# Performance work log

Hardware: AMD Instinct MI355X
Metric: run time of the kernel (lower is better)

## Reference

```python
import jax, jax.numpy as jnp
import numpy as np

NEG_INF = -9e15  # matches torch's -9000000000000000.0 mask value
ALPHA = 0.2      # LeakyReLU negative slope


def setup_inputs() -> dict:
    key = jax.random.key(0)
    k1, k2, k3, k4 = jax.random.split(key, 4)
    B, N, Fin, Fout, H = 32, 512, 256, 64, 8
    x = jax.random.normal(k1, (B, N, Fin), dtype=jnp.float32)
    adj = (jax.random.uniform(k2, (B, N, N)) < 0.5).astype(jnp.float32)
    # W: Linear(in_features, out_features*n_heads, bias=False) weight, stored as (Fin, Fout*H)
    W = jax.random.normal(k3, (Fin, Fout * H), dtype=jnp.float32) / np.sqrt(Fin).astype(np.float32)
    # a: attention vector per head over concat(src,dst) features -> (H, 2*Fout)
    a = jax.random.normal(k4, (H, 2 * Fout), dtype=jnp.float32) * 0.1
    return {"x": x, "adj": adj, "W": W, "a": a}


def reference(x, adj, W, a):
    # x: (B,N,Fin), adj: (B,N,N), W: (Fin, H*F), a: (H, 2F)
    B, N, _ = x.shape
    H, twoF = a.shape
    F = twoF // 2
    h = (x @ W).reshape(B, N, H, F)  # (B,N,H,F)
    # Decompose concat-score: e_ij = lrelu(h_i . a_src + h_j . a_dst) -- same math
    # as (cat(h_i,h_j) * a).sum(-1) without materializing (B,N,N,H,2F).
    s_src = jnp.einsum('bnhf,hf->bnh', h, a[:, :F])  # (B,N,H)
    s_dst = jnp.einsum('bnhf,hf->bnh', h, a[:, F:])  # (B,N,H)
    e = s_src[:, :, None, :] + s_dst[:, None, :, :]  # (B,N,N,H)
    e = jax.nn.leaky_relu(e, negative_slope=ALPHA)
    e = jnp.where(adj[..., None] > 0, e, NEG_INF)
    attn = jax.nn.softmax(e, axis=2)  # softmax over neighbors j (dim=2)
    # dropout omitted (eval mode / p effectively 0 for the reference baseline)
    h_prime = jnp.einsum('bijh,bjhf->bihf', attn, h)  # (B,N,H,F)
    return h_prime.reshape(B, N, H * F)  # concat=True
```

## Files before the change

kernel.cpp:

```cpp
#include <hip/hip_runtime.h>
#include <hip/hip_bf16.h>


#define ALPHA 0.2f

typedef __bf16 bf16x8 __attribute__((ext_vector_type(8)));
typedef __bf16 bf16x4 __attribute__((ext_vector_type(4)));
typedef float  f32x4  __attribute__((ext_vector_type(4)));

#define HT_STRIDE 520
#define WT_STRIDE 40

struct Smem {
    __bf16 hT[64][HT_STRIDE];
    __bf16 WT[64][WT_STRIDE];
    float  ssrc[512], sdst[512];
    float  rsum[256];
    float  asrc[64], adst[64];
};

__device__ inline bf16x8 ld8(const float* p) {
    float4 a0 = *(const float4*)p;
    float4 a1 = *(const float4*)(p + 4);
    bf16x8 r;
    r[0]=(__bf16)a0.x; r[1]=(__bf16)a0.y; r[2]=(__bf16)a0.z; r[3]=(__bf16)a0.w;
    r[4]=(__bf16)a1.x; r[5]=(__bf16)a1.y; r[6]=(__bf16)a1.z; r[7]=(__bf16)a1.w;
    return r;
}

__global__ __launch_bounds__(512, 4) void k_gat(const float* __restrict__ x,
                                                const float* __restrict__ adj,
                                                const float* __restrict__ W,
                                                const float* __restrict__ a,
                                                float* __restrict__ out) {
    __shared__ Smem sm;
    const int ihalf = blockIdx.x, h = blockIdx.y, b = blockIdx.z;
    const int tid  = threadIdx.x;
    const int wave = tid >> 6, lane = tid & 63;
    const int quad = lane >> 4, col = lane & 15;

    if (tid < 128) {
        float v = a[h * 128 + tid];
        if (tid < 64) sm.asrc[tid] = v; else sm.adst[tid - 64] = v;
    }

    {
        const float* xb = x + (long)b * 512 * 256;
        f32x4 acc[4][4] = {};
        const int c = tid & 63, kl = tid >> 6;
        for (int ks = 0; ks < 8; ++ks) {
            #pragma unroll
            for (int t = 0; t < 4; ++t)
                sm.WT[c][kl + t * 8] = (__bf16)W[(long)(ks * 32 + kl + t * 8) * 512 + h * 64 + c];
            __syncthreads();
            bf16x8 av[4], bv[4];
            #pragma unroll
            for (int it = 0; it < 4; ++it)
                av[it] = ld8(xb + (long)(wave * 64 + it * 16 + col) * 256 + ks * 32 + quad * 8);
            #pragma unroll
            for (int nt = 0; nt < 4; ++nt)
                bv[nt] = *(const bf16x8*)(&sm.WT[nt * 16 + col][quad * 8]);
            #pragma unroll
            for (int it = 0; it < 4; ++it)
                #pragma unroll
                for (int nt = 0; nt < 4; ++nt)
                    acc[it][nt] = __builtin_amdgcn_mfma_f32_16x16x32_bf16(av[it], bv[nt], acc[it][nt], 0, 0, 0);
            __syncthreads();
        }
        #pragma unroll
        for (int it = 0; it < 4; ++it)
            #pragma unroll
            for (int nt = 0; nt < 4; ++nt) {
                int f = nt * 16 + col;
                int j = wave * 64 + it * 16 + quad * 4;
                bf16x4 pk = { (__bf16)acc[it][nt][0], (__bf16)acc[it][nt][1],
                              (__bf16)acc[it][nt][2], (__bf16)acc[it][nt][3] };
                *(bf16x4*)(&sm.hT[f][j]) = pk;
            }
    }
    __syncthreads();

    {
        float as = 0.f, ad = 0.f;
        #pragma unroll 8
        for (int f = 0; f < 64; ++f) {
            float v = (float)sm.hT[f][tid];
            as += v * sm.asrc[f];
            ad += v * sm.adst[f];
        }
        sm.ssrc[tid] = as;
        sm.sdst[tid] = ad;
    }
    __syncthreads();

    {
        float si[2], sacc[2] = {0.f, 0.f};
        const float* arow[2];
        #pragma unroll
        for (int it = 0; it < 2; ++it) {
            int i = ihalf * 256 + wave * 32 + it * 16 + col;
            si[it]   = sm.ssrc[i & 511];
            arow[it] = adj + ((long)(b * 512 + i)) * 512;
        }
        f32x4 acc[2][4] = {};
        for (int ks = 0; ks < 16; ++ks) {
            int j0 = ks * 32 + quad * 8;
            f32x4 s0 = *(const f32x4*)&sm.sdst[j0];
            f32x4 s1 = *(const f32x4*)&sm.sdst[j0 + 4];
            float sd[8] = {s0[0],s0[1],s0[2],s0[3],s1[0],s1[1],s1[2],s1[3]};
            bf16x8 P[2];
            #pragma unroll
            for (int it = 0; it < 2; ++it) {
                float4 a0 = *(const float4*)(arow[it] + j0);
                float4 a1 = *(const float4*)(arow[it] + j0 + 4);
                float am[8] = {a0.x,a0.y,a0.z,a0.w,a1.x,a1.y,a1.z,a1.w};
                #pragma unroll
                for (int u = 0; u < 8; ++u) {
                    float e = si[it] + sd[u];
                    e = e > 0.f ? e : ALPHA * e;
                    float p = (am[u] > 0.f) ? __expf(e) : 0.f;
                    __bf16 pb = (__bf16)p;
                    sacc[it] += (float)pb;
                    P[it][u] = pb;
                }
            }
            #pragma unroll
            for (int nt = 0; nt < 4; ++nt) {
                bf16x8 bv = *(const bf16x8*)(&sm.hT[nt * 16 + col][j0]);
                #pragma unroll
                for (int it = 0; it < 2; ++it)
                    acc[it][nt] = __builtin_amdgcn_mfma_f32_16x16x32_bf16(P[it], bv, acc[it][nt], 0, 0, 0);
            }
        }
        #pragma unroll
        for (int it = 0; it < 2; ++it) {
            float s = sacc[it];
            s += __shfl_xor(s, 16);
            s += __shfl_xor(s, 32);
            if (quad == 0) sm.rsum[wave * 32 + it * 16 + col] = s;
        }
        __syncthreads();
        #pragma unroll
        for (int it = 0; it < 2; ++it)
            #pragma unroll
            for (int r = 0; r < 4; ++r) {
                int li = wave * 32 + it * 16 + quad * 4 + r;
                int i  = ihalf * 256 + li;
                float s = sm.rsum[li];
                float inv = (s > 0.f) ? 1.0f / s : 0.f;
                float* orow = out + ((long)(b * 512 + i)) * 512 + h * 64;
                #pragma unroll
                for (int nt = 0; nt < 4; ++nt)
                    orow[nt * 16 + col] = acc[it][nt][r] * inv;
            }
    }
}

extern "C" void kernel_launch(void* const* d_in, const int* in_sizes, int n_in,
                              void* d_out, int out_size, void* d_ws, size_t ws_size,
                              hipStream_t stream) {
    const float* x   = (const float*)d_in[0];
    const float* adj = (const float*)d_in[1];
    const float* W   = (const float*)d_in[2];
    const float* a   = (const float*)d_in[3];
    float* out = (float*)d_out;
    (void)d_ws; (void)ws_size;

    k_gat<<<dim3(2, 8, 32), 512, 0, stream>>>(x, adj, W, a, out);
}
```

Measured before the change: 161.0 us.

## Split GAT into projection and attention kernels through workspace, one block per head

Splits the fused kernel into two kernels. The first computes h = xW once per (batch, head), stores it transposed in bf16 in workspace, and folds the source and destination scores into the MFMA epilogue. The second loads h into XOR-swizzled shared memory and handles all 512 rows per block, where the old kernel recomputed the projection for each half of the rows. It also uses exp2 with prescaled scores, multiplies by the adjacency value instead of branching, and gets row sums from an MFMA against a ones vector. A fused fallback remains for small workspaces, and the split costs an extra launch plus roughly 17 MB of workspace traffic.

```diff
diff --git a/kernel.cpp b/kernel.cpp
--- a/kernel.cpp
+++ b/kernel.cpp
@@ -8,16 +8,13 @@
 typedef __bf16 bf16x4 __attribute__((ext_vector_type(4)));
 typedef float  f32x4  __attribute__((ext_vector_type(4)));
 
-#define HT_STRIDE 520
-#define WT_STRIDE 40
-
-struct Smem {
-    __bf16 hT[64][HT_STRIDE];
-    __bf16 WT[64][WT_STRIDE];
-    float  ssrc[512], sdst[512];
-    float  rsum[256];
-    float  asrc[64], adst[64];
-};
+#if __has_builtin(__builtin_amdgcn_exp2f)
+#define EXP2(x) __builtin_amdgcn_exp2f(x)
+#define ESCALE  1.4426950408889634f
+#else
+#define EXP2(x) __expf(x)
+#define ESCALE  1.0f
+#endif
 
 __device__ inline bf16x8 ld8(const float* p) {
     float4 a0 = *(const float4*)p;
@@ -28,44 +25,215 @@
     return r;
 }
 
-__global__ __launch_bounds__(512, 4) void k_gat(const float* __restrict__ x,
-                                                const float* __restrict__ adj,
-                                                const float* __restrict__ W,
-                                                const float* __restrict__ a,
-                                                float* __restrict__ out) {
-    __shared__ Smem sm;
-    const int ihalf = blockIdx.x, h = blockIdx.y, b = blockIdx.z;
-    const int tid  = threadIdx.x;
+#define WT_STRIDE 264
+__global__ __launch_bounds__(512) void k_h(const float* __restrict__ x,
+                                           const float* __restrict__ W,
+                                           const float* __restrict__ a,
+                                           __bf16* __restrict__ hT,
+                                           float* __restrict__ ssrc,
+                                           float* __restrict__ sdst) {
+    __shared__ __bf16 WT[64][WT_STRIDE];
+    const int h = blockIdx.x, b = blockIdx.y;
+    const int tid = threadIdx.x;
     const int wave = tid >> 6, lane = tid & 63;
     const int quad = lane >> 4, col = lane & 15;
-
+    const long bh = b * 8 + h;
+
+    {
+        int c = tid & 63, k0 = tid >> 6;
+        #pragma unroll 4
+        for (int t = 0; t < 32; ++t)
+            WT[c][k0 + t * 8] = (__bf16)W[(long)(k0 + t * 8) * 512 + h * 64 + c];
+    }
+    float asv[4], adv[4];
+    #pragma unroll
+    for (int nt = 0; nt < 4; ++nt) {
+        asv[nt] = a[h * 128 + nt * 16 + col];
+        adv[nt] = a[h * 128 + 64 + nt * 16 + col];
+    }
+    __syncthreads();
+
+    const float* xb = x + (long)b * 512 * 256;
+    f32x4 acc[4][4] = {};
+    for (int ks = 0; ks < 8; ++ks) {
+        int k0 = ks * 32 + quad * 8;
+        bf16x8 av[4], bv[4];
+        #pragma unroll
+        for (int it = 0; it < 4; ++it)
+            av[it] = ld8(xb + (long)(wave * 64 + it * 16 + col) * 256 + k0);
+        #pragma unroll
+        for (int nt = 0; nt < 4; ++nt)
+            bv[nt] = *(const bf16x8*)(&WT[nt * 16 + col][k0]);
+        #pragma unroll
+        for (int it = 0; it < 4; ++it)
+            #pragma unroll
+            for (int nt = 0; nt < 4; ++nt)
+                acc[it][nt] = __builtin_amdgcn_mfma_f32_16x16x32_bf16(av[it], bv[nt], acc[it][nt], 0, 0, 0);
+    }
+    #pragma unroll
+    for (int it = 0; it < 4; ++it)
+        #pragma unroll
+        for (int nt = 0; nt < 4; ++nt) {
+            int f = nt * 16 + col;
+            int j = wave * 64 + it * 16 + quad * 4;
+            bf16x4 pk = { (__bf16)acc[it][nt][0], (__bf16)acc[it][nt][1],
+                          (__bf16)acc[it][nt][2], (__bf16)acc[it][nt][3] };
+            *(bf16x4*)(hT + (bh * 64 + f) * 512 + j) = pk;
+        }
+    #pragma unroll
+    for (int it = 0; it < 4; ++it)
+        #pragma unroll
+        for (int r = 0; r < 4; ++r) {
+            float ps = 0.f, pd = 0.f;
+            #pragma unroll
+            for (int nt = 0; nt < 4; ++nt) {
+                ps += acc[it][nt][r] * asv[nt];
+                pd += acc[it][nt][r] * adv[nt];
+            }
+            #pragma unroll
+            for (int off = 1; off < 16; off <<= 1) {
+                ps += __shfl_xor(ps, off);
+                pd += __shfl_xor(pd, off);
+            }
+            if (col == 0) {
+                int j = wave * 64 + it * 16 + quad * 4 + r;
+                ssrc[bh * 512 + j] = ps * ESCALE;
+                sdst[bh * 512 + j] = pd * ESCALE;
+            }
+        }
+}
+
+__global__ __launch_bounds__(512, 4) void k_attn(const float* __restrict__ adj,
+                                                 const __bf16* __restrict__ hT,
+                                                 const float* __restrict__ ssrc,
+                                                 const float* __restrict__ sdst,
+                                                 float* __restrict__ out) {
+    __shared__ __bf16 hTs[64 * 512];
+    __shared__ float  sdsts[512], ssrcs[512];
+    const int h = blockIdx.x, b = blockIdx.y;
+    const int tid = threadIdx.x;
+    const int wave = tid >> 6, lane = tid & 63;
+    const int quad = lane >> 4, col = lane & 15;
+    const long bh = b * 8 + h;
+
+    {
+        int f = tid >> 3, c8 = tid & 7, s = f & 7;
+        const __bf16* src = hT + (bh * 64 + f) * 512;
+        #pragma unroll
+        for (int k = 0; k < 8; ++k) {
+            int blk = k * 8 + c8;
+            *(float4*)(&hTs[f * 512 + ((blk ^ s) * 8)]) = *(const float4*)(src + blk * 8);
+        }
+    }
+    ssrcs[tid] = ssrc[bh * 512 + tid];
+    sdsts[tid] = sdst[bh * 512 + tid];
+    __syncthreads();
+
+    float si[4];
+    const float* arow[4];
+    #pragma unroll
+    for (int it = 0; it < 4; ++it) {
+        int i = wave * 64 + it * 16 + col;
+        si[it]   = ssrcs[i];
+        arow[it] = adj + ((long)b * 512 + i) * 512;
+    }
+    bf16x8 ones;
+    #pragma unroll
+    for (int u = 0; u < 8; ++u) ones[u] = (__bf16)1.0f;
+
+    f32x4 acc[4][4] = {};
+    f32x4 accs[4]   = {};
+    for (int ks = 0; ks < 16; ++ks) {
+        int j0 = ks * 32 + quad * 8;
+        f32x4 s0 = *(const f32x4*)&sdsts[j0];
+        f32x4 s1 = *(const f32x4*)&sdsts[j0 + 4];
+        float sd[8] = {s0[0],s0[1],s0[2],s0[3],s1[0],s1[1],s1[2],s1[3]};
+        bf16x8 bv[4];
+        int sblk = ((ks * 4 + quad) ^ (col & 7)) * 8;
+        #pragma unroll
+        for (int nt = 0; nt < 4; ++nt)
+            bv[nt] = *(const bf16x8*)(&hTs[(nt * 16 + col) * 512 + sblk]);
+        bf16x8 P[4];
+        #pragma unroll
+        for (int it = 0; it < 4; ++it) {
+            float4 a0 = *(const float4*)(arow[it] + j0);
+            float4 a1 = *(const float4*)(arow[it] + j0 + 4);
+            float am[8] = {a0.x,a0.y,a0.z,a0.w,a1.x,a1.y,a1.z,a1.w};
+            #pragma unroll
+            for (int u = 0; u < 8; ++u) {
+                float e = si[it] + sd[u];
+                float l = fmaxf(e, ALPHA * e);
+                float p = am[u] * EXP2(l);
+                P[it][u] = (__bf16)p;
+            }
+        }
+        #pragma unroll
+        for (int it = 0; it < 4; ++it) {
+            #pragma unroll
+            for (int nt = 0; nt < 4; ++nt)
+                acc[it][nt] = __builtin_amdgcn_mfma_f32_16x16x32_bf16(P[it], bv[nt], acc[it][nt], 0, 0, 0);
+            accs[it] = __builtin_amdgcn_mfma_f32_16x16x32_bf16(P[it], ones, accs[it], 0, 0, 0);
+        }
+    }
+    #pragma unroll
+    for (int it = 0; it < 4; ++it)
+        #pragma unroll
+        for (int r = 0; r < 4; ++r) {
+            float s = accs[it][r];
+            float inv = (s > 0.f) ? 1.0f / s : 0.f;
+            int i = wave * 64 + it * 16 + quad * 4 + r;
+            float* orow = out + ((long)b * 512 + i) * 512 + h * 64;
+            #pragma unroll
+            for (int nt = 0; nt < 4; ++nt)
+                orow[nt * 16 + col] = acc[it][nt][r] * inv;
+        }
+}
+
+#define HT_STRIDE 520
+struct SmemF {
+    __bf16 hT[64][HT_STRIDE];
+    __bf16 WT[64][WT_STRIDE];
+    float  ssrc[512], sdst[512], rsum[512];
+    float  asrc[64], adst[64];
+};
+__global__ __launch_bounds__(512, 1) void k_gat_fused(const float* __restrict__ x,
+                                                      const float* __restrict__ adj,
+                                                      const float* __restrict__ W,
+                                                      const float* __restrict__ a,
+                                                      float* __restrict__ out) {
+    __shared__ SmemF sm;
+    const int h = blockIdx.x, b = blockIdx.y;
+    const int tid = threadIdx.x;
+    const int wave = tid >> 6, lane = tid & 63;
+    const int quad = lane >> 4, col = lane & 15;
     if (tid < 128) {
         float v = a[h * 128 + tid];
         if (tid < 64) sm.asrc[tid] = v; else sm.adst[tid - 64] = v;
     }
-
+    {
+        int c = tid & 63, k0 = tid >> 6;
+        #pragma unroll 4
+        for (int t = 0; t < 32; ++t)
+            sm.WT[c][k0 + t * 8] = (__bf16)W[(long)(k0 + t * 8) * 512 + h * 64 + c];
+    }
+    __syncthreads();
     {
         const float* xb = x + (long)b * 512 * 256;
         f32x4 acc[4][4] = {};
-        const int c = tid & 63, kl = tid >> 6;
         for (int ks = 0; ks < 8; ++ks) {
-            #pragma unroll
-            for (int t = 0; t < 4; ++t)
-                sm.WT[c][kl + t * 8] = (__bf16)W[(long)(ks * 32 + kl + t * 8) * 512 + h * 64 + c];
-            __syncthreads();
+            int k0 = ks * 32 + quad * 8;
             bf16x8 av[4], bv[4];
             #pragma unroll
             for (int it = 0; it < 4; ++it)
-                av[it] = ld8(xb + (long)(wave * 64 + it * 16 + col) * 256 + ks * 32 + quad * 8);
+                av[it] = ld8(xb + (long)(wave * 64 + it * 16 + col) * 256 + k0);
             #pragma unroll
             for (int nt = 0; nt < 4; ++nt)
-                bv[nt] = *(const bf16x8*)(&sm.WT[nt * 16 + col][quad * 8]);
+                bv[nt] = *(const bf16x8*)(&sm.WT[nt * 16 + col][k0]);
             #pragma unroll
             for (int it = 0; it < 4; ++it)
                 #pragma unroll
                 for (int nt = 0; nt < 4; ++nt)
                     acc[it][nt] = __builtin_amdgcn_mfma_f32_16x16x32_bf16(av[it], bv[nt], acc[it][nt], 0, 0, 0);
-            __syncthreads();
         }
         #pragma unroll
         for (int it = 0; it < 4; ++it)
@@ -79,7 +247,6 @@
             }
     }
     __syncthreads();
-
     {
         float as = 0.f, ad = 0.f;
         #pragma unroll 8
@@ -92,25 +259,24 @@
         sm.sdst[tid] = ad;
     }
     __syncthreads();
-
-    {
-        float si[2], sacc[2] = {0.f, 0.f};
-        const float* arow[2];
-        #pragma unroll
-        for (int it = 0; it < 2; ++it) {
-            int i = ihalf * 256 + wave * 32 + it * 16 + col;
-            si[it]   = sm.ssrc[i & 511];
+    {
+        float si[4], sacc[4] = {0.f, 0.f, 0.f, 0.f};
+        const float* arow[4];
+        #pragma unroll
+        for (int it = 0; it < 4; ++it) {
+            int i = wave * 64 + it * 16 + col;
+            si[it]   = sm.ssrc[i];
             arow[it] = adj + ((long)(b * 512 + i)) * 512;
         }
-        f32x4 acc[2][4] = {};
+        f32x4 acc[4][4] = {};
         for (int ks = 0; ks < 16; ++ks) {
             int j0 = ks * 32 + quad * 8;
             f32x4 s0 = *(const f32x4*)&sm.sdst[j0];
             f32x4 s1 = *(const f32x4*)&sm.sdst[j0 + 4];
             float sd[8] = {s0[0],s0[1],s0[2],s0[3],s1[0],s1[1],s1[2],s1[3]};
-            bf16x8 P[2];
-            #pragma unroll
-            for (int it = 0; it < 2; ++it) {
+            bf16x8 P[4];
+            #pragma unroll
+            for (int it = 0; it < 4; ++it) {
                 float4 a0 = *(const float4*)(arow[it] + j0);
                 float4 a1 = *(const float4*)(arow[it] + j0 + 4);
                 float am[8] = {a0.x,a0.y,a0.z,a0.w,a1.x,a1.y,a1.z,a1.w};
@@ -128,25 +294,24 @@
             for (int nt = 0; nt < 4; ++nt) {
                 bf16x8 bv = *(const bf16x8*)(&sm.hT[nt * 16 + col][j0]);
                 #pragma unroll
-                for (int it = 0; it < 2; ++it)
+                for (int it = 0; it < 4; ++it)
                     acc[it][nt] = __builtin_amdgcn_mfma_f32_16x16x32_bf16(P[it], bv, acc[it][nt], 0, 0, 0);
             }
         }
         #pragma unroll
-        for (int it = 0; it < 2; ++it) {
+        for (int it = 0; it < 4; ++it) {
             float s = sacc[it];
             s += __shfl_xor(s, 16);
             s += __shfl_xor(s, 32);
-            if (quad == 0) sm.rsum[wave * 32 + it * 16 + col] = s;
+            if (quad == 0) sm.rsum[wave * 64 + it * 16 + col] = s;
         }
         __syncthreads();
         #pragma unroll
-        for (int it = 0; it < 2; ++it)
+        for (int it = 0; it < 4; ++it)
             #pragma unroll
             for (int r = 0; r < 4; ++r) {
-                int li = wave * 32 + it * 16 + quad * 4 + r;
-                int i  = ihalf * 256 + li;
-                float s = sm.rsum[li];
+                int i = wave * 64 + it * 16 + quad * 4 + r;
+                float s = sm.rsum[i];
                 float inv = (s > 0.f) ? 1.0f / s : 0.f;
                 float* orow = out + ((long)(b * 512 + i)) * 512 + h * 64;
                 #pragma unroll
@@ -164,7 +329,15 @@
     const float* W   = (const float*)d_in[2];
     const float* a   = (const float*)d_in[3];
     float* out = (float*)d_out;
-    (void)d_ws; (void)ws_size;
-
-    k_gat<<<dim3(2, 8, 32), 512, 0, stream>>>(x, adj, W, a, out);
-}
+
+    const size_t WS_NEED = 16777216 + 2 * 524288;
+    if (ws_size >= WS_NEED) {
+        __bf16* hT   = (__bf16*)d_ws;
+        float*  ssrc = (float*)((char*)d_ws + 16777216);
+        float*  sdst = (float*)((char*)d_ws + 16777216 + 524288);
+        k_h   <<<dim3(8, 32), 512, 0, stream>>>(x, W, a, hT, ssrc, sdst);
+        k_attn<<<dim3(8, 32), 512, 0, stream>>>(adj, hT, ssrc, sdst, out);
+    } else {
+        k_gat_fused<<<dim3(8, 32), 512, 0, stream>>>(x, adj, W, a, out);
+    }
+}
```

Result: slower. 209.9 us (+30.4%).

## Merge row halves per block, preload W, prefetch adj, compute row sums via MFMA

Applied to the files above, without the earlier changes.

Each block now handles all 512 rows of one (batch, head) pair instead of half, so the projection x@W is computed once per pair rather than twice. All of W is staged into shared memory up front, which removes the per-k-step barriers. Adjacency loads are software-prefetched one step ahead. The exp is replaced by exp2 with a pre-scaled attention vector, the mask is applied by multiplying, and row sums come from an extra MFMA against a ones vector instead of shuffles plus a shared-memory pass. The grid shrinks to 256 blocks with launch bounds of 1, which lowers parallelism and raises register pressure.

```diff
diff --git a/kernel.cpp b/kernel.cpp
--- a/kernel.cpp
+++ b/kernel.cpp
@@ -2,20 +2,26 @@
 #include <hip/hip_bf16.h>
 
 
-#define ALPHA 0.2f
+#define ALPHA  0.2f
+#define ESCALE 1.4426950408889634f
 
 typedef __bf16 bf16x8 __attribute__((ext_vector_type(8)));
 typedef __bf16 bf16x4 __attribute__((ext_vector_type(4)));
 typedef float  f32x4  __attribute__((ext_vector_type(4)));
 
+#if __has_builtin(__builtin_amdgcn_exp2f)
+#define EXP2(x) __builtin_amdgcn_exp2f(x)
+#else
+#define EXP2(x) exp2f(x)
+#endif
+
 #define HT_STRIDE 520
-#define WT_STRIDE 40
+#define WT_STRIDE 264
 
 struct Smem {
     __bf16 hT[64][HT_STRIDE];
     __bf16 WT[64][WT_STRIDE];
     float  ssrc[512], sdst[512];
-    float  rsum[256];
     float  asrc[64], adst[64];
 };
 
@@ -28,44 +34,46 @@
     return r;
 }
 
-__global__ __launch_bounds__(512, 4) void k_gat(const float* __restrict__ x,
+__global__ __launch_bounds__(512, 1) void k_gat(const float* __restrict__ x,
                                                 const float* __restrict__ adj,
                                                 const float* __restrict__ W,
                                                 const float* __restrict__ a,
                                                 float* __restrict__ out) {
     __shared__ Smem sm;
-    const int ihalf = blockIdx.x, h = blockIdx.y, b = blockIdx.z;
+    const int b = blockIdx.x, h = blockIdx.y;
     const int tid  = threadIdx.x;
     const int wave = tid >> 6, lane = tid & 63;
     const int quad = lane >> 4, col = lane & 15;
 
     if (tid < 128) {
-        float v = a[h * 128 + tid];
+        float v = a[h * 128 + tid] * ESCALE;
         if (tid < 64) sm.asrc[tid] = v; else sm.adst[tid - 64] = v;
     }
+    {
+        int c = tid & 63, k0 = tid >> 6;
+        #pragma unroll 4
+        for (int t = 0; t < 32; ++t)
+            sm.WT[c][k0 + t * 8] = (__bf16)W[(long)(k0 + t * 8) * 512 + h * 64 + c];
+    }
+    __syncthreads();
 
     {
         const float* xb = x + (long)b * 512 * 256;
         f32x4 acc[4][4] = {};
-        const int c = tid & 63, kl = tid >> 6;
         for (int ks = 0; ks < 8; ++ks) {
-            #pragma unroll
-            for (int t = 0; t < 4; ++t)
-                sm.WT[c][kl + t * 8] = (__bf16)W[(long)(ks * 32 + kl + t * 8) * 512 + h * 64 + c];
-            __syncthreads();
+            int k0 = ks * 32 + quad * 8;
             bf16x8 av[4], bv[4];
             #pragma unroll
             for (int it = 0; it < 4; ++it)
-                av[it] = ld8(xb + (long)(wave * 64 + it * 16 + col) * 256 + ks * 32 + quad * 8);
+                av[it] = ld8(xb + (long)(wave * 64 + it * 16 + col) * 256 + k0);
             #pragma unroll
             for (int nt = 0; nt < 4; ++nt)
-                bv[nt] = *(const bf16x8*)(&sm.WT[nt * 16 + col][quad * 8]);
+                bv[nt] = *(const bf16x8*)(&sm.WT[nt * 16 + col][k0]);
             #pragma unroll
             for (int it = 0; it < 4; ++it)
                 #pragma unroll
                 for (int nt = 0; nt < 4; ++nt)
                     acc[it][nt] = __builtin_amdgcn_mfma_f32_16x16x32_bf16(av[it], bv[nt], acc[it][nt], 0, 0, 0);
-            __syncthreads();
         }
         #pragma unroll
         for (int it = 0; it < 4; ++it)
@@ -94,61 +102,76 @@
     __syncthreads();
 
     {
-        float si[2], sacc[2] = {0.f, 0.f};
-        const float* arow[2];
+        float si[4];
+        const float* arow[4];
         #pragma unroll
-        for (int it = 0; it < 2; ++it) {
-            int i = ihalf * 256 + wave * 32 + it * 16 + col;
-            si[it]   = sm.ssrc[i & 511];
-            arow[it] = adj + ((long)(b * 512 + i)) * 512;
+        for (int it = 0; it < 4; ++it) {
+            int i = wave * 64 + it * 16 + col;
+            si[it]   = sm.ssrc[i];
+            arow[it] = adj + ((long)b * 512 + i) * 512;
         }
-        f32x4 acc[2][4] = {};
+        bf16x8 ones;
+        #pragma unroll
+        for (int u = 0; u < 8; ++u) ones[u] = (__bf16)1.0f;
+
+        f32x4 acc[4][4] = {};
+        f32x4 accs[4]   = {};
+        float4 pa0[4], pa1[4];
+        #pragma unroll
+        for (int it = 0; it < 4; ++it) {
+            pa0[it] = *(const float4*)(arow[it] + quad * 8);
+            pa1[it] = *(const float4*)(arow[it] + quad * 8 + 4);
+        }
         for (int ks = 0; ks < 16; ++ks) {
             int j0 = ks * 32 + quad * 8;
             f32x4 s0 = *(const f32x4*)&sm.sdst[j0];
             f32x4 s1 = *(const f32x4*)&sm.sdst[j0 + 4];
             float sd[8] = {s0[0],s0[1],s0[2],s0[3],s1[0],s1[1],s1[2],s1[3]};
-            bf16x8 P[2];
+            float am[4][8];
             #pragma unroll
-            for (int it = 0; it < 2; ++it) {
-                float4 a0 = *(const float4*)(arow[it] + j0);
-                float4 a1 = *(const float4*)(arow[it] + j0 + 4);
-                float am[8] = {a0.x,a0.y,a0.z,a0.w,a1.x,a1.y,a1.z,a1.w};
+            for (int it = 0; it < 4; ++it) {
+                am[it][0]=pa0[it].x; am[it][1]=pa0[it].y;
+                am[it][2]=pa0[it].z; am[it][3]=pa0[it].w;
+                am[it][4]=pa1[it].x; am[it][5]=pa1[it].y;
+                am[it][6]=pa1[it].z; am[it][7]=pa1[it].w;
+            }
+            if (ks < 15) {
+                #pragma unroll
+                for (int it = 0; it < 4; ++it) {
+                    pa0[it] = *(const float4*)(arow[it] + j0 + 32);
+                    pa1[it] = *(const float4*)(arow[it] + j0 + 36);
+                }
+            }
+            bf16x8 P[4];
+            #pragma unroll
+            for (int it = 0; it < 4; ++it)
                 #pragma unroll
                 for (int u = 0; u < 8; ++u) {
                     float e = si[it] + sd[u];
-                    e = e > 0.f ? e : ALPHA * e;
-                    float p = (am[u] > 0.f) ? __expf(e) : 0.f;
-                    __bf16 pb = (__bf16)p;
-                    sacc[it] += (float)pb;
-                    P[it][u] = pb;
+                    float l = fmaxf(e, ALPHA * e);
+                    float p = am[it][u] * EXP2(l);
+                    P[it][u] = (__bf16)p;
                 }
-            }
+            bf16x8 bv[4];
             #pragma unroll
-            for (int nt = 0; nt < 4; ++nt) {
-                bf16x8 bv = *(const bf16x8*)(&sm.hT[nt * 16 + col][j0]);
+            for (int nt = 0; nt < 4; ++nt)
+                bv[nt] = *(const bf16x8*)(&sm.hT[nt * 16 + col][j0]);
+            #pragma unroll
+            for (int it = 0; it < 4; ++it) {
                 #pragma unroll
-                for (int it = 0; it < 2; ++it)
-                    acc[it][nt] = __builtin_amdgcn_mfma_f32_16x16x32_bf16(P[it], bv, acc[it][nt], 0, 0, 0);
+                for (int nt = 0; nt < 4; ++nt)
+                    acc[it][nt] = __builtin_amdgcn_mfma_f32_16x16x32_bf16(P[it], bv[nt], acc[it][nt], 0, 0, 0);
+                accs[it] = __builtin_amdgcn_mfma_f32_16x16x32_bf16(P[it], ones, accs[it], 0, 0, 0);
             }
         }
         #pragma unroll
-        for (int it = 0; it < 2; ++it) {
-            float s = sacc[it];
-            s += __shfl_xor(s, 16);
-            s += __shfl_xor(s, 32);
-            if (quad == 0) sm.rsum[wave * 32 + it * 16 + col] = s;
-        }
-        __syncthreads();
-        #pragma unroll
-        for (int it = 0; it < 2; ++it)
+        for (int it = 0; it < 4; ++it)
             #pragma unroll
             for (int r = 0; r < 4; ++r) {
-                int li = wave * 32 + it * 16 + quad * 4 + r;
-                int i  = ihalf * 256 + li;
-                float s = sm.rsum[li];
+                float s = accs[it][r];
                 float inv = (s > 0.f) ? 1.0f / s : 0.f;
-                float* orow = out + ((long)(b * 512 + i)) * 512 + h * 64;
+                int i = wave * 64 + it * 16 + quad * 4 + r;
+                float* orow = out + ((long)b * 512 + i) * 512 + h * 64;
                 #pragma unroll
                 for (int nt = 0; nt < 4; ++nt)
                     orow[nt * 16 + col] = acc[it][nt][r] * inv;
@@ -166,5 +189,5 @@
     float* out = (float*)d_out;
     (void)d_ws; (void)ws_size;
 
-    k_gat<<<dim3(2, 8, 32), 512, 0, stream>>>(x, adj, W, a, out);
+    k_gat<<<dim3(32, 8), 512, 0, stream>>>(x, adj, W, a, out);
 }
```

Measured after the change: 140.9 us. 12.5% less time.
